# Optimization experiments

Hardware: AMD Instinct MI355X
Metric: run time of the kernel (lower is better)

## Reference

```python
import jax, jax.numpy as jnp
import numpy as np

EMBED = 1024
HEADS = 16
HEAD_DIM = EMBED // HEADS
B, S = 2, 2048


def setup_inputs() -> dict:
    key = jax.random.key(0)
    k1, k2, k3 = jax.random.split(key, 3)
    scale = 1.0 / np.sqrt(EMBED)
    x = jax.random.normal(k1, (B, S, EMBED), dtype=jnp.float32)
    mask = jnp.ones((B, 1, 1, S), dtype=jnp.int32)
    Wqkv = jax.random.normal(k2, (3 * EMBED, EMBED), dtype=jnp.float32) * scale
    bqkv = jnp.zeros((3 * EMBED,), dtype=jnp.float32)
    Wout = jax.random.normal(k3, (EMBED, EMBED), dtype=jnp.float32) * scale
    bout = jnp.zeros((EMBED,), dtype=jnp.float32)
    return {"x": x, "mask": mask, "Wqkv": Wqkv, "bqkv": bqkv, "Wout": Wout, "bout": bout}


def reference(x, mask, Wqkv, bqkv, Wout, bout):
    Bsz, Sl, E = x.shape
    # fused QKV projection (torch Linear: x @ W.T + b)
    qkv = x @ Wqkv.T + bqkv                      # [B, S, 3E]
    qkv = qkv.reshape(Bsz, Sl, 3, HEADS, HEAD_DIM)
    qkv = jnp.transpose(qkv, (0, 2, 3, 1, 4))    # [B, 3, H, S, D]
    q, k, v = qkv[:, 0], qkv[:, 1], qkv[:, 2]    # each [B, H, S, D]
    scores = jnp.einsum("bhqd,bhkd->bhqk", q, k) / np.sqrt(HEAD_DIM)
    scores = jnp.where(mask == 0, -jnp.inf, scores)  # mask broadcasts [B,1,1,S]
    attn = jax.nn.softmax(scores, axis=-1)       # dropout is identity at eval
    out = jnp.einsum("bhqk,bhkd->bhqd", attn, v) # [B, H, S, D]
    out = jnp.transpose(out, (0, 2, 1, 3)).reshape(Bsz, Sl, E)
    return out @ Wout.T + bout
```

## Files before the change

### kernel.cpp

```cpp
#include <hip/hip_runtime.h>
#include <stdint.h>

typedef unsigned short u16;
typedef __bf16  bf16x8 __attribute__((ext_vector_type(8)));
typedef u16     u16x8  __attribute__((ext_vector_type(8)));
typedef u16     u16x4  __attribute__((ext_vector_type(4)));
typedef float   f32x4  __attribute__((ext_vector_type(4)));

#define MFMA16x16x32(a, b, c) __builtin_amdgcn_mfma_f32_16x16x32_bf16((a), (b), (c), 0, 0, 0)

__device__ __forceinline__ u16 f2bf(float f) {
  uint32_t u = __float_as_uint(f);
  u += 0x7FFFu + ((u >> 16) & 1u);
  return (u16)(u >> 16);
}

__device__ __forceinline__ uint32_t pktrunc(float a, float b) {
  return __builtin_amdgcn_perm(__float_as_uint(b), __float_as_uint(a), 0x07060302u);
}

__device__ __forceinline__ bf16x8 ldfrag(const u16* p) {
  return __builtin_bit_cast(bf16x8, *(const u16x8*)p);
}

__device__ __forceinline__ void gl2lds16(const u16* g, u16* l) {
  __builtin_amdgcn_global_load_lds(
      (__attribute__((address_space(1))) void*)g,
      (__attribute__((address_space(3))) void*)l, 16, 0, 0);
}

__global__ __launch_bounds__(256) void convert3(
    const float* __restrict__ x, const float* __restrict__ wq,
    const float* __restrict__ wo, u16* __restrict__ xb,
    u16* __restrict__ wqb, u16* __restrict__ wob) {
  const int NX = (4096 * 1024) / 8;
  const int NQ = (3072 * 1024) / 8;
  int i = blockIdx.x * 256 + threadIdx.x;
  const float* s;
  u16* d;
  if (i < NX)           { s = x;  d = xb;  }
  else if (i < NX + NQ) { s = wq; d = wqb; i -= NX; }
  else                  { s = wo; d = wob; i -= NX + NQ; }
  f32x4 a = ((const f32x4*)s)[2 * (size_t)i];
  f32x4 b = ((const f32x4*)s)[2 * (size_t)i + 1];
  u16x8 r;
  #pragma unroll
  for (int e = 0; e < 4; ++e) { r[e] = f2bf(a[e]); r[4 + e] = f2bf(b[e]); }
  ((u16x8*)d)[i] = r;
}

__global__ __launch_bounds__(256) void qkv_gemm(
    const u16* __restrict__ A, const u16* __restrict__ Bw,
    const float* __restrict__ bias, u16* __restrict__ Qo,
    u16* __restrict__ Ko, u16* __restrict__ Vo) {
  __shared__ __align__(16) u16 As[128 * 32];
  __shared__ __align__(16) u16 Bs[128 * 32];

  const int t = threadIdx.x;
  const int lane = t & 63, w = t >> 6;
  const int quad = lane >> 4, col = lane & 15;
  const int wm = w & 1, wn = w >> 1;
  const int m0 = blockIdx.y * 128, n0 = blockIdx.x * 128;

  f32x4 acc[4][4] = {};

  const int ar = t >> 2, ac = (t & 3) * 8;
  const u16* Ag0 = A + (size_t)(m0 + ar) * 1024 + ac;
  const u16* Ag1 = Ag0 + 64 * 1024;
  const u16* Bg0 = Bw + (size_t)(n0 + ar) * 1024 + ac;
  const u16* Bg1 = Bg0 + 64 * 1024;
  u16* Al0 = As + t * 8;
  u16* Al1 = As + 2048 + t * 8;
  u16* Bl0 = Bs + t * 8;
  u16* Bl1 = Bs + 2048 + t * 8;

  for (int kt = 0; kt < 32; ++kt) {
    const int ko = kt * 32;
    __syncthreads();
    gl2lds16(Ag0 + ko, Al0);
    gl2lds16(Ag1 + ko, Al1);
    gl2lds16(Bg0 + ko, Bl0);
    gl2lds16(Bg1 + ko, Bl1);
    __syncthreads();

    bf16x8 bfr[4];
    #pragma unroll
    for (int j = 0; j < 4; ++j)
      bfr[j] = ldfrag(Bs + (wn * 64 + j * 16 + col) * 32 + quad * 8);
    #pragma unroll
    for (int i = 0; i < 4; ++i) {
      bf16x8 afr = ldfrag(As + (wm * 64 + i * 16 + col) * 32 + quad * 8);
      #pragma unroll
      for (int j = 0; j < 4; ++j)
        acc[i][j] = MFMA16x16x32(afr, bfr[j], acc[i][j]);
    }
  }

  #pragma unroll
  for (int i = 0; i < 4; ++i) {
    const int m = m0 + wm * 64 + i * 16 + quad * 4;
    const int bb = m >> 11;
    const int s = m & 2047;
    #pragma unroll
    for (int j = 0; j < 4; ++j) {
      const int n = n0 + wn * 64 + j * 16 + col;
      const float bv = bias[n];
      const int which = n >> 10;
      const int h = (n >> 6) & 15;
      const int d = n & 63;
      u16* dst = (which == 0) ? Qo : ((which == 1) ? Ko : Vo);
      const float scale = (which == 0) ? 0.125f : 1.0f;
      const size_t base = ((size_t)(bb * 16 + h) * 2048 + s) * 64 + d;
      #pragma unroll
      for (int r = 0; r < 4; ++r)
        dst[base + (size_t)r * 64] = f2bf((acc[i][j][r] + bv) * scale);
    }
  }
}

__global__ __launch_bounds__(256) void transpose64(
    const u16* __restrict__ V, u16* __restrict__ Vt) {
  __shared__ u16 tile[64][72];
  const int t = threadIdx.x;
  const int s0 = blockIdx.x * 64;
  const int bh = blockIdx.y;
  const u16* Vb = V + (size_t)bh * (2048 * 64);
  u16* Vtb = Vt + (size_t)bh * (64 * 2048);
  #pragma unroll
  for (int p = 0; p < 2; ++p) {
    int c = t + 256 * p;
    int r = c >> 3, c8 = (c & 7) * 8;
    u16x8 v = *(const u16x8*)(Vb + (size_t)(s0 + r) * 64 + c8);
    #pragma unroll
    for (int e = 0; e < 8; ++e) tile[r][c8 + e] = v[e];
  }
  __syncthreads();
  #pragma unroll
  for (int p = 0; p < 2; ++p) {
    int c = t + 256 * p;
    int dr = c >> 3, c8 = (c & 7) * 8;
    u16x8 v;
    #pragma unroll
    for (int e = 0; e < 8; ++e) v[e] = tile[c8 + e][dr];
    *(u16x8*)(Vtb + (size_t)dr * 2048 + s0 + c8) = v;
  }
}

__global__ __launch_bounds__(512, 4) void attn(
    const u16* __restrict__ Q, const u16* __restrict__ K,
    const u16* __restrict__ Vt, const int* __restrict__ mask,
    u16* __restrict__ AO) {
  __shared__ __align__(16) u16 Ks[128 * 64];
  __shared__ __align__(16) u16 Vs[64 * 128];
  __shared__ __align__(16) u16 Ps[8][32 * 72];

  const int t = threadIdx.x;
  const int lane = t & 63, w = t >> 6;
  const int quad = lane >> 4, col = lane & 15;
  const int g = w & 1, u = w >> 1;
  const int qb = blockIdx.x, bh = blockIdx.y;
  const int b = bh >> 4, h = bh & 15;

  const u16* Qh = Q + (size_t)bh * (2048 * 64);
  const u16* Kh = K + (size_t)bh * (2048 * 64);
  const u16* Vh = Vt + (size_t)bh * (64 * 2048);
  const int* mb = mask + b * 2048;

  const int qw = qb * 128 + u * 32;
  const int keyg = g * 64;
  bf16x8 aQ[2][2];
  #pragma unroll
  for (int ct = 0; ct < 2; ++ct) {
    #pragma unroll
    for (int kh = 0; kh < 2; ++kh)
      aQ[ct][kh] = ldfrag(Qh + (size_t)(qw + ct * 16 + col) * 64 + kh * 32 + quad * 8);
  }

  f32x4 o[2][4] = {};
  float l[2] = {0.f, 0.f};
  u16* Pw = &Ps[w][0];

  for (int kb = 0; kb < 16; ++kb) {
    const int key0 = kb * 128;
    __syncthreads();
    #pragma unroll
    for (int p = 0; p < 2; ++p) {
      int c = t + 512 * p;
      int kr = c >> 3, kc = c & 7;
      gl2lds16(Kh + (size_t)(key0 + kr) * 64 + (kc ^ (kr & 7)) * 8, Ks + c * 8);
      int vr = c >> 4, vc = c & 15;
      gl2lds16(Vh + (size_t)vr * 2048 + key0 + (vc ^ (vr & 15)) * 8, Vs + c * 8);
    }
    __syncthreads();

    f32x4 sc[2][4] = {};
    #pragma unroll
    for (int j = 0; j < 4; ++j) {
      #pragma unroll
      for (int kh = 0; kh < 2; ++kh) {
        bf16x8 ak = ldfrag(Ks + (keyg + j * 16 + col) * 64 + (((kh * 4 + quad) ^ (col & 7)) * 8));
        sc[0][j] = MFMA16x16x32(ak, aQ[0][kh], sc[0][j]);
        sc[1][j] = MFMA16x16x32(ak, aQ[1][kh], sc[1][j]);
      }
    }

    #pragma unroll
    for (int jj = 0; jj < 4; ++jj) {
      int4 m4 = *(const int4*)(mb + key0 + keyg + jj * 16 + quad * 4);
      uint32_t M01 = (m4.x ? 0x0000FFFFu : 0u) | (m4.y ? 0xFFFF0000u : 0u);
      uint32_t M23 = (m4.z ? 0x0000FFFFu : 0u) | (m4.w ? 0xFFFF0000u : 0u);
      #pragma unroll
      for (int ct = 0; ct < 2; ++ct) {
        uint32_t pkA = pktrunc(__expf(sc[ct][jj][0]), __expf(sc[ct][jj][1])) & M01;
        uint32_t pkB = pktrunc(__expf(sc[ct][jj][2]), __expf(sc[ct][jj][3])) & M23;
        l[ct] += (__uint_as_float(pkA << 16) + __uint_as_float(pkA & 0xFFFF0000u)) +
                 (__uint_as_float(pkB << 16) + __uint_as_float(pkB & 0xFFFF0000u));
        uint2 pk; pk.x = pkA; pk.y = pkB;
        *(uint2*)(Pw + (ct * 16 + col) * 72 + jj * 16 + quad * 4) = pk;
      }
    }

    #pragma unroll
    for (int jp = 0; jp < 2; ++jp) {
      bf16x8 bP0 = ldfrag(Pw + col * 72 + jp * 32 + quad * 8);
      bf16x8 bP1 = ldfrag(Pw + (16 + col) * 72 + jp * 32 + quad * 8);
      #pragma unroll
      for (int dt = 0; dt < 4; ++dt) {
        bf16x8 av = ldfrag(Vs + (dt * 16 + col) * 128 + (((g * 8 + jp * 4 + quad) ^ col) * 8));
        o[0][dt] = MFMA16x16x32(av, bP0, o[0][dt]);
        o[1][dt] = MFMA16x16x32(av, bP1, o[1][dt]);
      }
    }
  }

  __syncthreads();
  float* Rb = (float*)(&Ps[0][0]);
  float* Ro = Rb + u * 2048 + lane * 32;
  float* Rl = Rb + 8192 + u * 128 + lane * 2;
  if (g == 1) {
    #pragma unroll
    for (int ct = 0; ct < 2; ++ct)
      #pragma unroll
      for (int dt = 0; dt < 4; ++dt)
        *(f32x4*)(Ro + ((ct * 4 + dt) ^ (lane & 7)) * 4) = o[ct][dt];
    Rl[0] = l[0]; Rl[1] = l[1];
  }
  __syncthreads();
  if (g == 0) {
    #pragma unroll
    for (int ct = 0; ct < 2; ++ct) {
      #pragma unroll
      for (int dt = 0; dt < 4; ++dt)
        o[ct][dt] += *(const f32x4*)(Ro + ((ct * 4 + dt) ^ (lane & 7)) * 4);
      float s = l[ct] + Rl[ct];
      s += __shfl_xor(s, 16);
      s += __shfl_xor(s, 32);
      l[ct] = 1.0f / s;
    }
    #pragma unroll
    for (int ct = 0; ct < 2; ++ct) {
      const int q = qw + ct * 16 + col;
      #pragma unroll
      for (int dt = 0; dt < 4; ++dt) {
        u16x4 v;
        #pragma unroll
        for (int r = 0; r < 4; ++r) v[r] = f2bf(o[ct][dt][r] * l[ct]);
        *(u16x4*)(AO + (size_t)(b * 2048 + q) * 1024 + h * 64 + dt * 16 + quad * 4) = v;
      }
    }
  }
}

__global__ __launch_bounds__(256) void proj_gemm(
    const u16* __restrict__ A, const u16* __restrict__ Bw,
    const float* __restrict__ bias, float* __restrict__ out) {
  __shared__ __align__(16) u16 As[128 * 32];
  __shared__ __align__(16) u16 Bs[128 * 32];

  const int t = threadIdx.x;
  const int lane = t & 63, w = t >> 6;
  const int quad = lane >> 4, col = lane & 15;
  const int wm = w & 1, wn = w >> 1;
  const int m0 = blockIdx.y * 128, n0 = blockIdx.x * 128;

  f32x4 acc[4][4] = {};

  const int ar = t >> 2, ac = (t & 3) * 8;
  const u16* Ag0 = A + (size_t)(m0 + ar) * 1024 + ac;
  const u16* Ag1 = Ag0 + 64 * 1024;
  const u16* Bg0 = Bw + (size_t)(n0 + ar) * 1024 + ac;
  const u16* Bg1 = Bg0 + 64 * 1024;
  u16* Al0 = As + t * 8;
  u16* Al1 = As + 2048 + t * 8;
  u16* Bl0 = Bs + t * 8;
  u16* Bl1 = Bs + 2048 + t * 8;

  for (int kt = 0; kt < 32; ++kt) {
    const int ko = kt * 32;
    __syncthreads();
    gl2lds16(Ag0 + ko, Al0);
    gl2lds16(Ag1 + ko, Al1);
    gl2lds16(Bg0 + ko, Bl0);
    gl2lds16(Bg1 + ko, Bl1);
    __syncthreads();

    bf16x8 bfr[4];
    #pragma unroll
    for (int j = 0; j < 4; ++j)
      bfr[j] = ldfrag(Bs + (wn * 64 + j * 16 + col) * 32 + quad * 8);
    #pragma unroll
    for (int i = 0; i < 4; ++i) {
      bf16x8 afr = ldfrag(As + (wm * 64 + i * 16 + col) * 32 + quad * 8);
      #pragma unroll
      for (int j = 0; j < 4; ++j)
        acc[i][j] = MFMA16x16x32(afr, bfr[j], acc[i][j]);
    }
  }

  #pragma unroll
  for (int i = 0; i < 4; ++i) {
    const int m = m0 + wm * 64 + i * 16 + quad * 4;
    #pragma unroll
    for (int j = 0; j < 4; ++j) {
      const int n = n0 + wn * 64 + j * 16 + col;
      const float bv = bias[n];
      #pragma unroll
      for (int r = 0; r < 4; ++r)
        out[(size_t)(m + r) * 1024 + n] = acc[i][j][r] + bv;
    }
  }
}

extern "C" void kernel_launch(void* const* d_in, const int* in_sizes, int n_in,
                              void* d_out, int out_size, void* d_ws, size_t ws_size,
                              hipStream_t stream) {
  (void)in_sizes; (void)n_in; (void)out_size; (void)ws_size;
  const float* x    = (const float*)d_in[0];
  const int*   mask = (const int*)d_in[1];
  const float* Wqkv = (const float*)d_in[2];
  const float* bqkv = (const float*)d_in[3];
  const float* Wout = (const float*)d_in[4];
  const float* bout = (const float*)d_in[5];
  float* out = (float*)d_out;
  char* ws = (char*)d_ws;

  u16* Xb  = (u16*)(ws);
  u16* Wqb = (u16*)(ws + ((size_t)8  << 20));
  u16* Wob = (u16*)(ws + ((size_t)14 << 20));
  u16* Qb  = (u16*)(ws + ((size_t)16 << 20));
  u16* Kb  = (u16*)(ws + ((size_t)24 << 20));
  u16* Vb  = (u16*)(ws + ((size_t)32 << 20));
  u16* Vtb = (u16*)(ws + ((size_t)40 << 20));
  u16* AO  = Xb;

  convert3<<<dim3(4096), dim3(256), 0, stream>>>(x, Wqkv, Wout, Xb, Wqb, Wob);
  qkv_gemm<<<dim3(24, 32), dim3(256), 0, stream>>>(Xb, Wqb, bqkv, Qb, Kb, Vb);
  transpose64<<<dim3(32, 32), dim3(256), 0, stream>>>(Vb, Vtb);
  attn<<<dim3(16, 32), dim3(512), 0, stream>>>(Qb, Kb, Vtb, mask, AO);
  proj_gemm<<<dim3(8, 32), dim3(256), 0, stream>>>(AO, Wob, bout, out);
}
```

Measured before the change: 208.5 us.

## Widen GEMM K-tile with swizzled LDS, vectorize epilogues, compute softmax sum via MFMA

Both GEMMs now stage a 64-wide K slice per iteration into XOR-swizzled LDS, which halves the barrier count and is meant to avoid bank conflicts. They also swap the MFMA operand order so each lane owns four consecutive output columns, allowing vectorized bias loads and 8-byte or 16-byte stores instead of scalar scattered stores. In attention, the row sum of P is computed with an extra MFMA against a ones vector rather than scalar adds and cross-lane shuffles, and the P buffer stride changes from 72 to 68 with split 8-byte loads. The cost is extra MFMA work and more LDS per GEMM block, which may reduce occupancy.

```diff
diff --git a/kernel.cpp b/kernel.cpp
--- a/kernel.cpp
+++ b/kernel.cpp
@@ -2,10 +2,11 @@
 #include <stdint.h>
 
 typedef unsigned short u16;
-typedef __bf16  bf16x8 __attribute__((ext_vector_type(8)));
-typedef u16     u16x8  __attribute__((ext_vector_type(8)));
-typedef u16     u16x4  __attribute__((ext_vector_type(4)));
-typedef float   f32x4  __attribute__((ext_vector_type(4)));
+typedef __bf16    bf16x8 __attribute__((ext_vector_type(8)));
+typedef u16       u16x8  __attribute__((ext_vector_type(8)));
+typedef u16       u16x4  __attribute__((ext_vector_type(4)));
+typedef float     f32x4  __attribute__((ext_vector_type(4)));
+typedef uint32_t  u32x4  __attribute__((ext_vector_type(4)));
 
 #define MFMA16x16x32(a, b, c) __builtin_amdgcn_mfma_f32_16x16x32_bf16((a), (b), (c), 0, 0, 0)
 
@@ -21,6 +22,13 @@
 
 __device__ __forceinline__ bf16x8 ldfrag(const u16* p) {
   return __builtin_bit_cast(bf16x8, *(const u16x8*)p);
+}
+
+__device__ __forceinline__ bf16x8 ldfrag2(const u16* p) {
+  uint2 a = *(const uint2*)p;
+  uint2 b = *(const uint2*)(p + 4);
+  u32x4 t; t[0] = a.x; t[1] = a.y; t[2] = b.x; t[3] = b.y;
+  return __builtin_bit_cast(bf16x8, t);
 }
 
 __device__ __forceinline__ void gl2lds16(const u16* g, u16* l) {
@@ -53,8 +61,8 @@
     const u16* __restrict__ A, const u16* __restrict__ Bw,
     const float* __restrict__ bias, u16* __restrict__ Qo,
     u16* __restrict__ Ko, u16* __restrict__ Vo) {
-  __shared__ __align__(16) u16 As[128 * 32];
-  __shared__ __align__(16) u16 Bs[128 * 32];
+  __shared__ __align__(16) u16 As[128 * 64];
+  __shared__ __align__(16) u16 Bs[128 * 64];
 
   const int t = threadIdx.x;
   const int lane = t & 63, w = t >> 6;
@@ -64,56 +72,53 @@
 
   f32x4 acc[4][4] = {};
 
-  const int ar = t >> 2, ac = (t & 3) * 8;
-  const u16* Ag0 = A + (size_t)(m0 + ar) * 1024 + ac;
-  const u16* Ag1 = Ag0 + 64 * 1024;
-  const u16* Bg0 = Bw + (size_t)(n0 + ar) * 1024 + ac;
-  const u16* Bg1 = Bg0 + 64 * 1024;
-  u16* Al0 = As + t * 8;
-  u16* Al1 = As + 2048 + t * 8;
-  u16* Bl0 = Bs + t * 8;
-  u16* Bl1 = Bs + 2048 + t * 8;
-
-  for (int kt = 0; kt < 32; ++kt) {
-    const int ko = kt * 32;
-    __syncthreads();
-    gl2lds16(Ag0 + ko, Al0);
-    gl2lds16(Ag1 + ko, Al1);
-    gl2lds16(Bg0 + ko, Bl0);
-    gl2lds16(Bg1 + ko, Bl1);
-    __syncthreads();
-
-    bf16x8 bfr[4];
-    #pragma unroll
-    for (int j = 0; j < 4; ++j)
-      bfr[j] = ldfrag(Bs + (wn * 64 + j * 16 + col) * 32 + quad * 8);
+  for (int kt = 0; kt < 16; ++kt) {
+    const int ko = kt * 64;
+    __syncthreads();
+    #pragma unroll
+    for (int p = 0; p < 4; ++p) {
+      int c = t + 256 * p;
+      int r = c >> 3, cc = c & 7;
+      int so = ko + ((cc ^ (r & 7)) * 8);
+      gl2lds16(A  + (size_t)(m0 + r) * 1024 + so, As + c * 8);
+      gl2lds16(Bw + (size_t)(n0 + r) * 1024 + so, Bs + c * 8);
+    }
+    __syncthreads();
+
+    #pragma unroll
+    for (int kk = 0; kk < 2; ++kk) {
+      const int e8 = ((kk * 4 + quad) ^ (col & 7)) * 8;
+      bf16x8 bfr[4];
+      #pragma unroll
+      for (int j = 0; j < 4; ++j)
+        bfr[j] = ldfrag(Bs + (wn * 64 + j * 16 + col) * 64 + e8);
+      #pragma unroll
+      for (int i = 0; i < 4; ++i) {
+        bf16x8 afr = ldfrag(As + (wm * 64 + i * 16 + col) * 64 + e8);
+        #pragma unroll
+        for (int j = 0; j < 4; ++j)
+          acc[i][j] = MFMA16x16x32(bfr[j], afr, acc[i][j]);
+      }
+    }
+  }
+
+  const int nb = n0 + wn * 64;
+  const int which = nb >> 10;
+  const int h = (nb >> 6) & 15;
+  u16* dst = (which == 0) ? Qo : ((which == 1) ? Ko : Vo);
+  const float scale = (which == 0) ? 0.125f : 1.0f;
+
+  #pragma unroll
+  for (int j = 0; j < 4; ++j) {
+    const f32x4 b4 = *(const f32x4*)(bias + nb + j * 16 + quad * 4);
     #pragma unroll
     for (int i = 0; i < 4; ++i) {
-      bf16x8 afr = ldfrag(As + (wm * 64 + i * 16 + col) * 32 + quad * 8);
-      #pragma unroll
-      for (int j = 0; j < 4; ++j)
-        acc[i][j] = MFMA16x16x32(afr, bfr[j], acc[i][j]);
-    }
-  }
-
-  #pragma unroll
-  for (int i = 0; i < 4; ++i) {
-    const int m = m0 + wm * 64 + i * 16 + quad * 4;
-    const int bb = m >> 11;
-    const int s = m & 2047;
-    #pragma unroll
-    for (int j = 0; j < 4; ++j) {
-      const int n = n0 + wn * 64 + j * 16 + col;
-      const float bv = bias[n];
-      const int which = n >> 10;
-      const int h = (n >> 6) & 15;
-      const int d = n & 63;
-      u16* dst = (which == 0) ? Qo : ((which == 1) ? Ko : Vo);
-      const float scale = (which == 0) ? 0.125f : 1.0f;
-      const size_t base = ((size_t)(bb * 16 + h) * 2048 + s) * 64 + d;
-      #pragma unroll
-      for (int r = 0; r < 4; ++r)
-        dst[base + (size_t)r * 64] = f2bf((acc[i][j][r] + bv) * scale);
+      const int m = m0 + wm * 64 + i * 16 + col;
+      const int bb = m >> 11, s = m & 2047;
+      u16x4 vv;
+      #pragma unroll
+      for (int r = 0; r < 4; ++r) vv[r] = f2bf((acc[i][j][r] + b4[r]) * scale);
+      *(u16x4*)(dst + ((size_t)(bb * 16 + h) * 2048 + s) * 64 + j * 16 + quad * 4) = vv;
     }
   }
 }
@@ -152,7 +157,7 @@
     u16* __restrict__ AO) {
   __shared__ __align__(16) u16 Ks[128 * 64];
   __shared__ __align__(16) u16 Vs[64 * 128];
-  __shared__ __align__(16) u16 Ps[8][32 * 72];
+  __shared__ __align__(16) u16 Ps[8][32 * 68];
 
   const int t = threadIdx.x;
   const int lane = t & 63, w = t >> 6;
@@ -166,6 +171,11 @@
   const u16* Vh = Vt + (size_t)bh * (64 * 2048);
   const int* mb = mask + b * 2048;
 
+  u16x8 ou;
+  #pragma unroll
+  for (int e = 0; e < 8; ++e) ou[e] = 0x3F80;
+  const bf16x8 ones = __builtin_bit_cast(bf16x8, ou);
+
   const int qw = qb * 128 + u * 32;
   const int keyg = g * 64;
   bf16x8 aQ[2][2];
@@ -177,7 +187,7 @@
   }
 
   f32x4 o[2][4] = {};
-  float l[2] = {0.f, 0.f};
+  f32x4 lacc[2] = {};
   u16* Pw = &Ps[w][0];
 
   for (int kb = 0; kb < 16; ++kb) {
@@ -211,19 +221,19 @@
       uint32_t M23 = (m4.z ? 0x0000FFFFu : 0u) | (m4.w ? 0xFFFF0000u : 0u);
       #pragma unroll
       for (int ct = 0; ct < 2; ++ct) {
-        uint32_t pkA = pktrunc(__expf(sc[ct][jj][0]), __expf(sc[ct][jj][1])) & M01;
-        uint32_t pkB = pktrunc(__expf(sc[ct][jj][2]), __expf(sc[ct][jj][3])) & M23;
-        l[ct] += (__uint_as_float(pkA << 16) + __uint_as_float(pkA & 0xFFFF0000u)) +
-                 (__uint_as_float(pkB << 16) + __uint_as_float(pkB & 0xFFFF0000u));
-        uint2 pk; pk.x = pkA; pk.y = pkB;
-        *(uint2*)(Pw + (ct * 16 + col) * 72 + jj * 16 + quad * 4) = pk;
+        uint2 pk;
+        pk.x = pktrunc(__expf(sc[ct][jj][0]), __expf(sc[ct][jj][1])) & M01;
+        pk.y = pktrunc(__expf(sc[ct][jj][2]), __expf(sc[ct][jj][3])) & M23;
+        *(uint2*)(Pw + (ct * 16 + col) * 68 + jj * 16 + quad * 4) = pk;
       }
     }
 
     #pragma unroll
     for (int jp = 0; jp < 2; ++jp) {
-      bf16x8 bP0 = ldfrag(Pw + col * 72 + jp * 32 + quad * 8);
-      bf16x8 bP1 = ldfrag(Pw + (16 + col) * 72 + jp * 32 + quad * 8);
+      bf16x8 bP0 = ldfrag2(Pw + col * 68 + jp * 32 + quad * 8);
+      bf16x8 bP1 = ldfrag2(Pw + (16 + col) * 68 + jp * 32 + quad * 8);
+      lacc[0] = MFMA16x16x32(ones, bP0, lacc[0]);
+      lacc[1] = MFMA16x16x32(ones, bP1, lacc[1]);
       #pragma unroll
       for (int dt = 0; dt < 4; ++dt) {
         bf16x8 av = ldfrag(Vs + (dt * 16 + col) * 128 + (((g * 8 + jp * 4 + quad) ^ col) * 8));
@@ -243,19 +253,17 @@
       #pragma unroll
       for (int dt = 0; dt < 4; ++dt)
         *(f32x4*)(Ro + ((ct * 4 + dt) ^ (lane & 7)) * 4) = o[ct][dt];
-    Rl[0] = l[0]; Rl[1] = l[1];
+    Rl[0] = lacc[0][0]; Rl[1] = lacc[1][0];
   }
   __syncthreads();
   if (g == 0) {
+    float rl[2];
     #pragma unroll
     for (int ct = 0; ct < 2; ++ct) {
       #pragma unroll
       for (int dt = 0; dt < 4; ++dt)
         o[ct][dt] += *(const f32x4*)(Ro + ((ct * 4 + dt) ^ (lane & 7)) * 4);
-      float s = l[ct] + Rl[ct];
-      s += __shfl_xor(s, 16);
-      s += __shfl_xor(s, 32);
-      l[ct] = 1.0f / s;
+      rl[ct] = 1.0f / (lacc[ct][0] + Rl[ct]);
     }
     #pragma unroll
     for (int ct = 0; ct < 2; ++ct) {
@@ -264,7 +272,7 @@
       for (int dt = 0; dt < 4; ++dt) {
         u16x4 v;
         #pragma unroll
-        for (int r = 0; r < 4; ++r) v[r] = f2bf(o[ct][dt][r] * l[ct]);
+        for (int r = 0; r < 4; ++r) v[r] = f2bf(o[ct][dt][r] * rl[ct]);
         *(u16x4*)(AO + (size_t)(b * 2048 + q) * 1024 + h * 64 + dt * 16 + quad * 4) = v;
       }
     }
@@ -274,8 +282,8 @@
 __global__ __launch_bounds__(256) void proj_gemm(
     const u16* __restrict__ A, const u16* __restrict__ Bw,
     const float* __restrict__ bias, float* __restrict__ out) {
-  __shared__ __align__(16) u16 As[128 * 32];
-  __shared__ __align__(16) u16 Bs[128 * 32];
+  __shared__ __align__(16) u16 As[128 * 64];
+  __shared__ __align__(16) u16 Bs[128 * 64];
 
   const int t = threadIdx.x;
   const int lane = t & 63, w = t >> 6;
@@ -285,48 +293,45 @@
 
   f32x4 acc[4][4] = {};
 
-  const int ar = t >> 2, ac = (t & 3) * 8;
-  const u16* Ag0 = A + (size_t)(m0 + ar) * 1024 + ac;
-  const u16* Ag1 = Ag0 + 64 * 1024;
-  const u16* Bg0 = Bw + (size_t)(n0 + ar) * 1024 + ac;
-  const u16* Bg1 = Bg0 + 64 * 1024;
-  u16* Al0 = As + t * 8;
-  u16* Al1 = As + 2048 + t * 8;
-  u16* Bl0 = Bs + t * 8;
-  u16* Bl1 = Bs + 2048 + t * 8;
-
-  for (int kt = 0; kt < 32; ++kt) {
-    const int ko = kt * 32;
-    __syncthreads();
-    gl2lds16(Ag0 + ko, Al0);
-    gl2lds16(Ag1 + ko, Al1);
-    gl2lds16(Bg0 + ko, Bl0);
-    gl2lds16(Bg1 + ko, Bl1);
-    __syncthreads();
-
-    bf16x8 bfr[4];
-    #pragma unroll
-    for (int j = 0; j < 4; ++j)
-      bfr[j] = ldfrag(Bs + (wn * 64 + j * 16 + col) * 32 + quad * 8);
+  for (int kt = 0; kt < 16; ++kt) {
+    const int ko = kt * 64;
+    __syncthreads();
+    #pragma unroll
+    for (int p = 0; p < 4; ++p) {
+      int c = t + 256 * p;
+      int r = c >> 3, cc = c & 7;
+      int so = ko + ((cc ^ (r & 7)) * 8);
+      gl2lds16(A  + (size_t)(m0 + r) * 1024 + so, As + c * 8);
+      gl2lds16(Bw + (size_t)(n0 + r) * 1024 + so, Bs + c * 8);
+    }
+    __syncthreads();
+
+    #pragma unroll
+    for (int kk = 0; kk < 2; ++kk) {
+      const int e8 = ((kk * 4 + quad) ^ (col & 7)) * 8;
+      bf16x8 bfr[4];
+      #pragma unroll
+      for (int j = 0; j < 4; ++j)
+        bfr[j] = ldfrag(Bs + (wn * 64 + j * 16 + col) * 64 + e8);
+      #pragma unroll
+      for (int i = 0; i < 4; ++i) {
+        bf16x8 afr = ldfrag(As + (wm * 64 + i * 16 + col) * 64 + e8);
+        #pragma unroll
+        for (int j = 0; j < 4; ++j)
+          acc[i][j] = MFMA16x16x32(bfr[j], afr, acc[i][j]);
+      }
+    }
+  }
+
+  const int nb = n0 + wn * 64;
+  #pragma unroll
+  for (int j = 0; j < 4; ++j) {
+    const f32x4 b4 = *(const f32x4*)(bias + nb + j * 16 + quad * 4);
     #pragma unroll
     for (int i = 0; i < 4; ++i) {
-      bf16x8 afr = ldfrag(As + (wm * 64 + i * 16 + col) * 32 + quad * 8);
-      #pragma unroll
-      for (int j = 0; j < 4; ++j)
-        acc[i][j] = MFMA16x16x32(afr, bfr[j], acc[i][j]);
-    }
-  }
-
-  #pragma unroll
-  for (int i = 0; i < 4; ++i) {
-    const int m = m0 + wm * 64 + i * 16 + quad * 4;
-    #pragma unroll
-    for (int j = 0; j < 4; ++j) {
-      const int n = n0 + wn * 64 + j * 16 + col;
-      const float bv = bias[n];
-      #pragma unroll
-      for (int r = 0; r < 4; ++r)
-        out[(size_t)(m + r) * 1024 + n] = acc[i][j][r] + bv;
+      const int m = m0 + wm * 64 + i * 16 + col;
+      f32x4 vv = acc[i][j] + b4;
+      *(f32x4*)(out + (size_t)m * 1024 + nb + j * 16 + quad * 4) = vv;
     }
   }
 }
```

New measurement: 204.4 us. -2.0%, faster.
